# Kernel optimization log

Hardware: AMD Instinct MI355X
Metric: run time of the kernel (lower is better)

Reference implementation:

```python
import jax, jax.numpy as jnp
import numpy as np

THRESHOLD = 0.5

def _conv(x, w, b):
    y = jax.lax.conv_general_dilated(x, w, (1, 1), 'SAME',
                                     dimension_numbers=('NCHW', 'OIHW', 'NCHW'))
    return y + b[None, :, None, None]

def _gather2d(img, iy, ix):
    # img [B,C,H,W], iy/ix [B,h,w] int -> [B,C,h,w]
    return jax.vmap(lambda im, y, x: im[:, y, x])(img, iy, ix)

def _grid_sample_bilinear(img, grid):
    # torch F.grid_sample(mode='bilinear', padding_mode='border', align_corners=False)
    # img [B,C,H,W], grid [B,h,w,2] with (x,y) in [-1,1]
    B, C, H, W = img.shape
    x = (grid[..., 0] + 1.0) * (W * 0.5) - 0.5
    y = (grid[..., 1] + 1.0) * (H * 0.5) - 0.5
    x0 = jnp.floor(x); y0 = jnp.floor(y)
    wx = (x - x0)[:, None, :, :]; wy = (y - y0)[:, None, :, :]
    x0i = jnp.clip(x0.astype(jnp.int32), 0, W - 1)
    x1i = jnp.clip(x0.astype(jnp.int32) + 1, 0, W - 1)
    y0i = jnp.clip(y0.astype(jnp.int32), 0, H - 1)
    y1i = jnp.clip(y0.astype(jnp.int32) + 1, 0, H - 1)
    v00 = _gather2d(img, y0i, x0i); v01 = _gather2d(img, y0i, x1i)
    v10 = _gather2d(img, y1i, x0i); v11 = _gather2d(img, y1i, x1i)
    return (v00 * (1 - wx) * (1 - wy) + v01 * wx * (1 - wy)
            + v10 * (1 - wx) * wy + v11 * wx * wy)

def _encoder(lr, w_in, b_in, res_w, res_b):
    x = _conv(lr, w_in, b_in)
    for i in range(res_w.shape[0]):  # small fixed layer count
        r = _conv(jax.nn.relu(_conv(x, res_w[i, 0], res_b[i, 0])), res_w[i, 1], res_b[i, 1])
        x = x + r
    return x  # [B,64,Hl,Wl]

def _make_inp(feat, coord, cell):
    # nearest-sampled feature + relative coord + scaled cell (LIIF-style make_inp)
    B, C, Hl, Wl = feat.shape
    y = (coord[..., 0] + 1.0) * (Hl * 0.5) - 0.5
    x = (coord[..., 1] + 1.0) * (Wl * 0.5) - 0.5
    iyn = jnp.clip(jnp.floor(y + 0.5).astype(jnp.int32), 0, Hl - 1)
    ixn = jnp.clip(jnp.floor(x + 0.5).astype(jnp.int32), 0, Wl - 1)
    fs = _gather2d(feat, iyn, ixn).transpose(0, 2, 3, 1)  # [B,h,w,C]
    cy = (2.0 * iyn + 1.0) / Hl - 1.0
    cx = (2.0 * ixn + 1.0) / Wl - 1.0
    rel = jnp.stack([(coord[..., 0] - cy) * Hl, (coord[..., 1] - cx) * Wl], axis=-1)
    cell_s = cell * jnp.array([Hl, Wl], dtype=cell.dtype)
    return jnp.concatenate([fs, rel, cell_s], axis=-1)  # [B,h,w,C+4]

def setup_inputs() -> dict:
    key = jax.random.key(0)
    ks = jax.random.split(key, 16)
    B, Hl, Wl, h, w, C = 2, 96, 96, 384, 384, 64
    lr = jax.random.normal(ks[0], (B, 3, Hl, Wl), jnp.float32)
    ys = (jnp.arange(h, dtype=jnp.float32) + 0.5) / h * 2.0 - 1.0
    xs = (jnp.arange(w, dtype=jnp.float32) + 0.5) / w * 2.0 - 1.0
    gy, gx = jnp.meshgrid(ys, xs, indexing='ij')
    coord = jnp.broadcast_to(jnp.stack([gy, gx], -1), (B, h, w, 2))  # (y,x)
    cell = jnp.broadcast_to(jnp.array([2.0 / h, 2.0 / w], jnp.float32), (B, h, w, 2))
    def lin(k, fan_in, shape):
        return jax.random.normal(k, shape, jnp.float32) / np.sqrt(fan_in)
    D = C + 4  # 68
    return {
        'lr': lr, 'coord': coord, 'cell': cell,
        'enc_w_in': jax.random.normal(ks[1], (C, 3, 3, 3), jnp.float32) * 0.05,
        'enc_b_in': jnp.zeros((C,), jnp.float32),
        'enc_res_w': jax.random.normal(ks[2], (4, 2, C, C, 3, 3), jnp.float32) * 0.02,
        'enc_res_b': jnp.zeros((4, 2, C), jnp.float32),
        'cls_w1': lin(ks[3], D, (D, 64)), 'cls_b1': jnp.zeros((64,), jnp.float32),
        'cls_w2': lin(ks[4], 64, (64, 2)), 'cls_b2': jnp.zeros((2,), jnp.float32),
        'lw1': lin(ks[5], D, (D, 64)), 'lb1': jnp.zeros((64,), jnp.float32),
        'lw2': lin(ks[6], 64, (64, 64)), 'lb2': jnp.zeros((64,), jnp.float32),
        'lw3': lin(ks[7], 64, (64, 3)), 'lb3': jnp.zeros((3,), jnp.float32),
        'hw1': lin(ks[8], D, (D, 256)), 'hb1': jnp.zeros((256,), jnp.float32),
        'hmid_w': lin(ks[9], 256, (2, 256, 256)), 'hmid_b': jnp.zeros((2, 256), jnp.float32),
        'hw_out': lin(ks[10], 256, (256, 3)), 'hb_out': jnp.zeros((3,), jnp.float32),
    }

def reference(lr, coord, cell, enc_w_in, enc_b_in, enc_res_w, enc_res_b,
              cls_w1, cls_b1, cls_w2, cls_b2,
              lw1, lb1, lw2, lb2, lw3, lb3,
              hw1, hb1, hmid_w, hmid_b, hw_out, hb_out):
    feat = _encoder(lr, enc_w_in, enc_b_in, enc_res_w, enc_res_b)
    inp = _make_inp(feat, coord, cell)  # [B,h,w,68]
    # classifier -> softmax difficulty gate
    logits = jax.nn.relu(inp @ cls_w1 + cls_b1) @ cls_w2 + cls_b2
    diff = jax.nn.softmax(logits, axis=-1)
    hard = diff[..., 1] > THRESHOLD  # [B,h,w]
    # light sampler (dense over all pixels; where-select == gather/scatter dispatch)
    pl = jax.nn.relu(inp @ lw1 + lb1)
    pl = jax.nn.relu(pl @ lw2 + lb2)
    pl = pl @ lw3 + lb3
    # heavy sampler
    ph = jax.nn.relu(inp @ hw1 + hb1)
    for i in range(hmid_w.shape[0]):
        ph = jax.nn.relu(ph @ hmid_w[i] + hmid_b[i])
    ph = ph @ hw_out + hb_out
    pred = jnp.where(hard[..., None], ph, pl)  # [B,h,w,3]
    pred = pred.transpose(0, 3, 1, 2)  # [B,3,h,w]
    pred = pred + _grid_sample_bilinear(lr, coord[..., ::-1])  # coord.flip(-1) -> (x,y)
    ratio_easy = jnp.mean(1.0 - hard.astype(jnp.float32))
    return (pred, ratio_easy)
```

## Files before the change

kernel.cpp:

```cpp
#include <hip/hip_runtime.h>

#define HL 96
#define WL 96
#define HO 384
#define WO 384
#define NPIX (2*HO*WO)
#define FEAT_ELEMS ((size_t)2*64*HL*WL)
#define PLANE (HL*WL)

typedef unsigned short us4 __attribute__((ext_vector_type(4)));
typedef unsigned short us8 __attribute__((ext_vector_type(8)));
typedef __bf16         b8  __attribute__((ext_vector_type(8)));
typedef float          f32x4 __attribute__((ext_vector_type(4)));

__device__ __forceinline__ unsigned short f2b(float x) {
  unsigned u = __builtin_bit_cast(unsigned, x);
  unsigned r = (u + 0x7FFFu + ((u >> 16) & 1u)) >> 16;
  return (unsigned short)r;
}

__device__ __forceinline__ f32x4 MF(us8 a, us8 b, f32x4 c) {
  return __builtin_amdgcn_mfma_f32_16x16x32_bf16(
      __builtin_bit_cast(b8, a), __builtin_bit_cast(b8, b), c, 0, 0, 0);
}

template<int CIN, int COPT, bool RELU, bool RES>
__global__ __launch_bounds__(256) void conv_s_k(
    const float* __restrict__ in, const float* __restrict__ wP,
    const float* __restrict__ bias, const float* __restrict__ res,
    float* __restrict__ out)
{
  const int t   = threadIdx.x;
  const int p   = blockIdx.x * 256 + t;
  const int co0 = blockIdx.y * COPT;
  const int b   = blockIdx.z;
  const int x   = p % WL;
  const bool xl = (x == 0), xr = (x == WL - 1);

  float acc[COPT];
  #pragma unroll
  for (int j = 0; j < COPT; ++j) acc[j] = bias[co0 + j];

  int  ic[3]; bool yv[3];
  int  im[3], ip[3];
  #pragma unroll
  for (int ky = 0; ky < 3; ++ky) {
    int pr = p + (ky - 1) * WL;
    yv[ky] = ((unsigned)pr < (unsigned)PLANE);
    ic[ky] = yv[ky] ? pr : 0;
    im[ky] = ic[ky] - 1; if (im[ky] < 0) im[ky] = 0;
    ip[ky] = ic[ky] + 1; if (ip[ky] > PLANE - 1) ip[ky] = PLANE - 1;
  }

  const float* inb = in + (size_t)b * CIN * PLANE;

  #pragma unroll 2
  for (int ci = 0; ci < CIN; ++ci) {
    const float* pl = inb + (size_t)ci * PLANE;
    #pragma unroll
    for (int ky = 0; ky < 3; ++ky) {
      float am = pl[im[ky]];
      float a0 = pl[ic[ky]];
      float ap = pl[ip[ky]];
      if (!yv[ky]) { am = 0.f; a0 = 0.f; ap = 0.f; }
      if (xl) am = 0.f;
      if (xr) ap = 0.f;
      const float* wrow = wP + (size_t)(ci * 9 + ky * 3) * 64 + co0;
      #pragma unroll
      for (int j = 0; j < COPT; ++j) acc[j] += am * wrow[j];
      #pragma unroll
      for (int j = 0; j < COPT; ++j) acc[j] += a0 * wrow[64 + j];
      #pragma unroll
      for (int j = 0; j < COPT; ++j) acc[j] += ap * wrow[128 + j];
    }
  }

  size_t ob = ((size_t)b * 64 + co0) * PLANE + p;
  #pragma unroll
  for (int j = 0; j < COPT; ++j) {
    float v = acc[j];
    if (RELU) v = fmaxf(v, 0.f);
    if (RES)  v += res[ob + (size_t)j * PLANE];
    out[ob + (size_t)j * PLANE] = v;
  }
}

__global__ __launch_bounds__(256) void prep_convw_k(const float* __restrict__ src,
                                                    float* __restrict__ dst, int cin)
{
  int idx = blockIdx.x * 256 + threadIdx.x;
  int tot = cin * 9 * 64;
  if (idx >= tot) return;
  int co = idx % 64; int r = idx / 64;
  int ci = r / 9, tap = r % 9;
  dst[idx] = src[((size_t)co * cin + ci) * 9 + tap];
}

__global__ __launch_bounds__(256) void nchw_to_nhwc_k(const float* __restrict__ in,
                                                      float* __restrict__ out)
{
  __shared__ float s[64][65];
  const int b = blockIdx.y;
  const int pix0 = blockIdx.x * 64;
  const int t = threadIdx.x;
  #pragma unroll
  for (int cc = 0; cc < 16; ++cc) {
    int co = cc * 4 + (t >> 6);
    int px = t & 63;
    s[px][co] = in[((size_t)b * 64 + co) * PLANE + pix0 + px];
  }
  __syncthreads();
  #pragma unroll
  for (int pp = 0; pp < 16; ++pp) {
    int px = pp * 4 + (t >> 6);
    int co = t & 63;
    out[((size_t)b * PLANE + pix0 + px) * 64 + co] = s[px][co];
  }
}

__global__ __launch_bounds__(256) void prep_wt_k(const float* __restrict__ src,
    unsigned short* __restrict__ dst, int K, int N, int Kpad, int Npad)
{
  int idx = blockIdx.x * 256 + threadIdx.x;
  if (idx >= Kpad * Npad) return;
  int n = idx / Kpad, k = idx - n * Kpad;
  float v = (k < K && n < N) ? src[(size_t)k * N + n] : 0.f;
  dst[idx] = f2b(v);
}

template<int NT, int KT>
__device__ __forceinline__ void mfma_compute(
    const unsigned short* __restrict__ aBase, int AS,
    const unsigned short* __restrict__ WT, int Kpad,
    int n0, int lane, f32x4 (&acc)[4][NT])
{
  const int lr = lane & 15;
  const int lc = lane >> 4;
  #pragma unroll
  for (int m = 0; m < 4; ++m)
    #pragma unroll
    for (int j = 0; j < NT; ++j) acc[m][j] = (f32x4){0.f, 0.f, 0.f, 0.f};

  const unsigned short* aP = aBase + lr * AS + lc * 8;
  const unsigned short* bP = WT + (size_t)(n0 + lr) * Kpad + lc * 8;

  constexpr int KCH = (KT >= 4) ? 4 : KT;
  #pragma unroll
  for (int kc = 0; kc < KT; kc += KCH) {
    us8 breg[KCH][NT];
    #pragma unroll
    for (int kk = 0; kk < KCH; ++kk)
      #pragma unroll
      for (int j = 0; j < NT; ++j)
        breg[kk][j] = *(const us8*)(bP + (size_t)j * 16 * Kpad + (kc + kk) * 32);
    #pragma unroll
    for (int kc2 = 0; kc2 < KCH; ++kc2) {
      us8 a0[4];
      #pragma unroll
      for (int m = 0; m < 4; ++m)
        a0[m] = *(const us8*)(aP + (m * 16) * AS + (kc + kc2) * 32);
      #pragma unroll
      for (int m = 0; m < 4; ++m)
        #pragma unroll
        for (int j = 0; j < NT; ++j)
          acc[m][j] = MF(a0[m], breg[kc2][j], acc[m][j]);
    }
  }
}

template<int NT, bool RELU>
__device__ __forceinline__ void mfma_store(
    const f32x4 (&acc)[4][NT], const float* __restrict__ bias,
    unsigned short* __restrict__ dBase, int DS, int dCol0, int n0, int lane)
{
  const int lr = lane & 15;
  const int lc = lane >> 4;
  #pragma unroll
  for (int j = 0; j < NT; ++j) {
    int n = n0 + j * 16 + lr;
    float bv = bias[n];
    #pragma unroll
    for (int m = 0; m < 4; ++m)
      #pragma unroll
      for (int r = 0; r < 4; ++r) {
        float v = acc[m][j][r] + bv;
        if (RELU) v = fmaxf(v, 0.f);
        dBase[(m * 16 + lc * 4 + r) * DS + dCol0 + n] = f2b(v);
      }
  }
}

template<int KT>
__device__ __forceinline__ void mfma_out3w(
    const unsigned short* __restrict__ aBase, int AS,
    const unsigned short* __restrict__ WT, int Kpad,
    const float* __restrict__ bias, float (*dst)[4], int mtile, int lane)
{
  const int lr = lane & 15;
  const int lc = lane >> 4;
  f32x4 acc = (f32x4){0.f, 0.f, 0.f, 0.f};
  const unsigned short* aP = aBase + (mtile * 16 + lr) * AS + lc * 8;
  const unsigned short* bP = WT + (size_t)lr * Kpad + lc * 8;

  constexpr int KCH = (KT >= 4) ? 4 : KT;
  #pragma unroll
  for (int kc = 0; kc < KT; kc += KCH) {
    us8 breg[KCH];
    #pragma unroll
    for (int kk = 0; kk < KCH; ++kk)
      breg[kk] = *(const us8*)(bP + (kc + kk) * 32);
    #pragma unroll
    for (int kk = 0; kk < KCH; ++kk) {
      us8 a = *(const us8*)(aP + (kc + kk) * 32);
      acc = MF(a, breg[kk], acc);
    }
  }
  if (lr < 3) {
    float bv = bias[lr];
    #pragma unroll
    for (int r = 0; r < 4; ++r)
      dst[mtile * 16 + lc * 4 + r][lr] = acc[r] + bv;
  }
}

__device__ __forceinline__ void nearest_idx(float gy, float gx, int& iy, int& ix)
{
  float fy = (gy + 1.f) * (HL * 0.5f) - 0.5f;
  float fx = (gx + 1.f) * (WL * 0.5f) - 0.5f;
  iy = min(max((int)floorf(fy + 0.5f), 0), HL - 1);
  ix = min(max((int)floorf(fx + 0.5f), 0), WL - 1);
}

__device__ __forceinline__ float bilinear_lr(const float* __restrict__ lrimg,
                                             int b, int ch, float gy, float gx)
{
  float x = (gx + 1.f) * (WL * 0.5f) - 0.5f;
  float y = (gy + 1.f) * (HL * 0.5f) - 0.5f;
  float xf = floorf(x), yf = floorf(y);
  float wx = x - xf, wy = y - yf;
  int x0i = min(max((int)xf,     0), WL - 1);
  int x1i = min(max((int)xf + 1, 0), WL - 1);
  int y0i = min(max((int)yf,     0), HL - 1);
  int y1i = min(max((int)yf + 1, 0), HL - 1);
  const float* img = lrimg + ((size_t)b * 3 + ch) * PLANE;
  float v00 = img[y0i * WL + x0i], v01 = img[y0i * WL + x1i];
  float v10 = img[y1i * WL + x0i], v11 = img[y1i * WL + x1i];
  return v00 * (1.f - wx) * (1.f - wy) + v01 * wx * (1.f - wy)
       + v10 * (1.f - wx) * wy + v11 * wx * wy;
}

template<int JB>
__device__ __forceinline__ void cls_block(
    const float* __restrict__ fp,
    float e0, float e1, float e2, float e3,
    const float* __restrict__ cw1, const float* __restrict__ cb1,
    const float* __restrict__ cw2,
    int j0, float& l0, float& l1)
{
  float acc[JB];
  #pragma unroll
  for (int j = 0; j < JB; ++j) acc[j] = cb1[j0 + j];
  #pragma unroll 4
  for (int kq = 0; kq < 16; ++kq) {
    float4 a4 = *(const float4*)(fp + kq * 4);
    float av[4] = {a4.x, a4.y, a4.z, a4.w};
    #pragma unroll
    for (int kk = 0; kk < 4; ++kk) {
      const float* wr = cw1 + (size_t)(kq * 4 + kk) * 64 + j0;
      float a = av[kk];
      #pragma unroll
      for (int j = 0; j < JB; ++j) acc[j] += a * wr[j];
    }
  }
  {
    const float* wr = cw1 + (size_t)64 * 64 + j0;
    #pragma unroll
    for (int j = 0; j < JB; ++j) acc[j] += e0 * wr[j];
    wr += 64;
    #pragma unroll
    for (int j = 0; j < JB; ++j) acc[j] += e1 * wr[j];
    wr += 64;
    #pragma unroll
    for (int j = 0; j < JB; ++j) acc[j] += e2 * wr[j];
    wr += 64;
    #pragma unroll
    for (int j = 0; j < JB; ++j) acc[j] += e3 * wr[j];
  }
  #pragma unroll
  for (int j = 0; j < JB; ++j) {
    float h = fmaxf(acc[j], 0.f);
    l0 += h * cw2[(j0 + j) * 2 + 0];
    l1 += h * cw2[(j0 + j) * 2 + 1];
  }
}

__global__ __launch_bounds__(256, 4) void cls_gate_k(
    const float* __restrict__ featT, const float* __restrict__ coord,
    const float* __restrict__ cell,
    const float* __restrict__ cw1, const float* __restrict__ cb1,
    const float* __restrict__ cw2, const float* __restrict__ cb2,
    int* __restrict__ counters, unsigned* __restrict__ easyList,
    unsigned* __restrict__ hardList)
{
  const int g = blockIdx.x * 256 + threadIdx.x;
  const int b = g / (HO * WO);
  const float gy = coord[(size_t)g * 2 + 0];
  const float gx = coord[(size_t)g * 2 + 1];
  int iy, ix; nearest_idx(gy, gx, iy, ix);
  const float* fp = featT + (((size_t)b * PLANE) + iy * WL + ix) * 64;

  float cy = (2.f * iy + 1.f) / HL - 1.f;
  float cx = (2.f * ix + 1.f) / WL - 1.f;
  float e0 = (gy - cy) * HL;
  float e1 = (gx - cx) * WL;
  float e2 = cell[(size_t)g * 2 + 0] * HL;
  float e3 = cell[(size_t)g * 2 + 1] * WL;

  float l0 = cb2[0], l1 = cb2[1];
  cls_block<32>(fp, e0, e1, e2, e3, cw1, cb1, cw2, 0,  l0, l1);
  cls_block<32>(fp, e0, e1, e2, e3, cw1, cb1, cw2, 32, l0, l1);
  bool hard = (l1 > l0);

  unsigned long long mh = __ballot(hard);
  int lane = threadIdx.x & 63;
  int nh = __popcll(mh);
  int baseH = 0, baseE = 0;
  if (lane == 0) {
    baseH = atomicAdd(&counters[1], nh);
    baseE = atomicAdd(&counters[0], 64 - nh);
  }
  baseH = __shfl(baseH, 0);
  baseE = __shfl(baseE, 0);
  unsigned long long below = (1ull << lane) - 1ull;
  int hb = __popcll(mh & below);
  if (hard) hardList[baseH + hb] = (unsigned)g;
  else      easyList[baseE + (lane - hb)] = (unsigned)g;
}

__device__ __forceinline__ void build_inp_row(
    const float* __restrict__ featT, const float* __restrict__ coord,
    const float* __restrict__ cell, unsigned g, int p, int q8,
    unsigned short (*sInpB)[104])
{
  int b = g / (HO * WO);
  float gy = coord[(size_t)g * 2 + 0];
  float gx = coord[(size_t)g * 2 + 1];
  int iy, ix; nearest_idx(gy, gx, iy, ix);
  const float* fpt = featT + (((size_t)b * PLANE) + iy * WL + ix) * 64 + q8 * 8;
  float4 u0 = *(const float4*)fpt;
  float4 u1 = *(const float4*)(fpt + 4);
  us8 pk;
  pk[0]=f2b(u0.x); pk[1]=f2b(u0.y); pk[2]=f2b(u0.z); pk[3]=f2b(u0.w);
  pk[4]=f2b(u1.x); pk[5]=f2b(u1.y); pk[6]=f2b(u1.z); pk[7]=f2b(u1.w);
  *(us8*)&sInpB[p][q8 * 8] = pk;
  if (q8 == 0) {
    float cy = (2.f * iy + 1.f) / HL - 1.f;
    float cx = (2.f * ix + 1.f) / WL - 1.f;
    float e0 = (gy - cy) * HL, e1 = (gx - cx) * WL;
    float e2 = cell[(size_t)g * 2 + 0] * HL, e3 = cell[(size_t)g * 2 + 1] * WL;
    us4 pe; pe[0]=f2b(e0); pe[1]=f2b(e1); pe[2]=f2b(e2); pe[3]=f2b(e3);
    *(us4*)&sInpB[p][64] = pe;
  }
  if (q8 == 1) {
    us4 z = (us4){0,0,0,0};
    #pragma unroll
    for (int c = 0; c < 9; ++c) *(us4*)&sInpB[p][68 + c * 4] = z;
  }
}

__global__ __launch_bounds__(256, 4) void light_k(
    const float* __restrict__ featT, const float* __restrict__ coord,
    const float* __restrict__ cell,  const float* __restrict__ lrimg,
    const float* __restrict__ lb1, const float* __restrict__ lb2,
    const float* __restrict__ lb3,
    const unsigned short* __restrict__ lw1T, const unsigned short* __restrict__ lw2T,
    const unsigned short* __restrict__ lw3T,
    const int* __restrict__ counters, const unsigned* __restrict__ list,
    float* __restrict__ out)
{
  const int nE = counters[0];
  const int g0 = blockIdx.x * 64;
  if (g0 >= nE) return;

  __shared__ unsigned short sInpB[64][104];
  __shared__ unsigned short sL1[64][72];
  __shared__ unsigned short sL2[64][72];
  __shared__ float sP[64][4];
  __shared__ unsigned sIdx[64];

  const int t = threadIdx.x, lane = t & 63, w = t >> 6;

  {
    const int p = t >> 2, q = t & 3;
    int i = g0 + p; if (i > nE - 1) i = nE - 1;
    unsigned g = list[i];
    if (q == 0) sIdx[p] = g;
    build_inp_row(featT, coord, cell, g, p, q * 2,     sInpB);
    build_inp_row(featT, coord, cell, g, p, q * 2 + 1, sInpB);
  }
  __syncthreads();

  { f32x4 acc[4][1];
    mfma_compute<1, 3>(&sInpB[0][0], 104, lw1T, 96, w * 16, lane, acc);
    mfma_store<1, true>(acc, lb1, &sL1[0][0], 72, 0, w * 16, lane); }
  __syncthreads();
  { f32x4 acc[4][1];
    mfma_compute<1, 2>(&sL1[0][0], 72, lw2T, 64, w * 16, lane, acc);
    mfma_store<1, true>(acc, lb2, &sL2[0][0], 72, 0, w * 16, lane); }
  __syncthreads();
  mfma_out3w<2>(&sL2[0][0], 72, lw3T, 64, lb3, sP, w, lane);
  __syncthreads();

  if (t < 192) {
    int p = t / 3, ch = t % 3;
    int i = g0 + p;
    if (i < nE) {
      unsigned g = sIdx[p];
      int b = g / (HO * WO);
      int rem = g % (HO * WO);
      int oy = rem / WO, ox = rem % WO;
      float gy = coord[(size_t)g * 2 + 0];
      float gx = coord[(size_t)g * 2 + 1];
      float v = bilinear_lr(lrimg, b, ch, gy, gx);
      out[(((size_t)b * 3 + ch) * HO + oy) * WO + ox] = sP[p][ch] + v;
    }
  }
}

__global__ __launch_bounds__(512, 4) void heavy_k(
    const float* __restrict__ featT, const float* __restrict__ coord,
    const float* __restrict__ cell,  const float* __restrict__ lrimg,
    const float* __restrict__ hb1, const float* __restrict__ hmb,
    const float* __restrict__ hbo,
    const unsigned short* __restrict__ hw1T, const unsigned short* __restrict__ hm0T,
    const unsigned short* __restrict__ hm1T, const unsigned short* __restrict__ hwoT,
    const int* __restrict__ counters, const unsigned* __restrict__ list,
    float* __restrict__ out)
{
  const int nH = counters[1];
  const int g0 = blockIdx.x * 64;
  if (g0 >= nH) return;

  __shared__ unsigned short sAct[64][264];
  __shared__ unsigned short sInpB[64][104];
  __shared__ float sP[64][4];
  __shared__ unsigned sIdx[64];

  const int t = threadIdx.x, lane = t & 63, w = t >> 6;

  {
    const int p = t >> 3, q = t & 7;
    int i = g0 + p; if (i > nH - 1) i = nH - 1;
    unsigned g = list[i];
    if (q == 0) sIdx[p] = g;
    build_inp_row(featT, coord, cell, g, p, q, sInpB);
  }
  __syncthreads();

  { f32x4 acc[4][2];
    mfma_compute<2, 3>(&sInpB[0][0], 104, hw1T, 96, w * 32, lane, acc);
    mfma_store<2, true>(acc, hb1, &sAct[0][0], 264, 0, w * 32, lane); }
  __syncthreads();
  { f32x4 acc[4][2];
    mfma_compute<2, 8>(&sAct[0][0], 264, hm0T, 256, w * 32, lane, acc);
    __syncthreads();
    mfma_store<2, true>(acc, hmb, &sAct[0][0], 264, 0, w * 32, lane); }
  __syncthreads();
  { f32x4 acc[4][2];
    mfma_compute<2, 8>(&sAct[0][0], 264, hm1T, 256, w * 32, lane, acc);
    __syncthreads();
    mfma_store<2, true>(acc, hmb + 256, &sAct[0][0], 264, 0, w * 32, lane); }
  __syncthreads();
  if (w < 4) mfma_out3w<8>(&sAct[0][0], 264, hwoT, 256, hbo, sP, w, lane);
  __syncthreads();

  if (t < 192) {
    int p = t / 3, ch = t % 3;
    int i = g0 + p;
    if (i < nH) {
      unsigned g = sIdx[p];
      int b = g / (HO * WO);
      int rem = g % (HO * WO);
      int oy = rem / WO, ox = rem % WO;
      float gy = coord[(size_t)g * 2 + 0];
      float gx = coord[(size_t)g * 2 + 1];
      float v = bilinear_lr(lrimg, b, ch, gy, gx);
      out[(((size_t)b * 3 + ch) * HO + oy) * WO + ox] = sP[p][ch] + v;
    }
  }
}

__global__ void finalize_k(const int* __restrict__ counters, float* __restrict__ out)
{
  out[(size_t)NPIX * 3] = (float)(counters[0]) / (float)NPIX;
}

extern "C" void kernel_launch(void* const* d_in, const int* in_sizes, int n_in,
                              void* d_out, int out_size, void* d_ws, size_t ws_size,
                              hipStream_t stream)
{
  const float* lr       = (const float*)d_in[0];
  const float* coord    = (const float*)d_in[1];
  const float* cell     = (const float*)d_in[2];
  const float* enc_w_in = (const float*)d_in[3];
  const float* enc_b_in = (const float*)d_in[4];
  const float* enc_rw   = (const float*)d_in[5];
  const float* enc_rb   = (const float*)d_in[6];
  const float* cw1      = (const float*)d_in[7];
  const float* cb1      = (const float*)d_in[8];
  const float* cw2      = (const float*)d_in[9];
  const float* cb2      = (const float*)d_in[10];
  const float* lw1      = (const float*)d_in[11];
  const float* lb1      = (const float*)d_in[12];
  const float* lw2      = (const float*)d_in[13];
  const float* lb2      = (const float*)d_in[14];
  const float* lw3      = (const float*)d_in[15];
  const float* lb3      = (const float*)d_in[16];
  const float* hw1      = (const float*)d_in[17];
  const float* hb1      = (const float*)d_in[18];
  const float* hmw      = (const float*)d_in[19];
  const float* hmb      = (const float*)d_in[20];
  const float* hwo      = (const float*)d_in[21];
  const float* hbo      = (const float*)d_in[22];
  float* out = (float*)d_out;

  char* ws = (char*)d_ws;
  float* xA    = (float*)(ws + 1024);
  float* tmp   = xA  + FEAT_ELEMS;
  float* xB    = tmp + FEAT_ELEMS;
  float* featT = tmp;
  unsigned short* wb = (unsigned short*)(xB + FEAT_ELEMS);
  unsigned short* lw1T = wb;
  unsigned short* lw2T = lw1T + 64*96;
  unsigned short* lw3T = lw2T + 64*64;
  unsigned short* hw1T = lw3T + 16*64;
  unsigned short* hm0T = hw1T + 256*96;
  unsigned short* hm1T = hm0T + 65536;
  unsigned short* hwoT = hm1T + 65536;
  const size_t nb16 = 64*96 + 64*64 + 16*64 + 256*96 + 2*65536 + 16*256;
  float* cwIn  = (float*)(wb + nb16);
  float* cwRes = cwIn + 1728;
  size_t need = 1024 + 3 * FEAT_ELEMS * sizeof(float)
              + nb16 * 2 + (1728 + 8 * 36864) * sizeof(float);
  if (ws_size < need) return;

  int*      counters = (int*)xB;
  unsigned* easyList = (unsigned*)(xB + 16);
  unsigned* hardList = easyList + NPIX;

  auto prep = [&](const float* s, unsigned short* d, int K, int N, int Kp, int Np) {
    int tot = Kp * Np;
    prep_wt_k<<<(tot + 255) / 256, 256, 0, stream>>>(s, d, K, N, Kp, Np);
  };
  prep(lw1, lw1T, 68, 64, 96, 64);
  prep(lw2, lw2T, 64, 64, 64, 64);
  prep(lw3, lw3T, 64, 3, 64, 16);
  prep(hw1, hw1T, 68, 256, 96, 256);
  prep(hmw,         hm0T, 256, 256, 256, 256);
  prep(hmw + 65536, hm1T, 256, 256, 256, 256);
  prep(hwo, hwoT, 256, 3, 256, 16);

  prep_convw_k<<<(1728 + 255) / 256, 256, 0, stream>>>(enc_w_in, cwIn, 3);
  for (int l = 0; l < 8; ++l)
    prep_convw_k<<<(36864 + 255) / 256, 256, 0, stream>>>(
        enc_rw + (size_t)l * 36864, cwRes + (size_t)l * 36864, 64);

  dim3 cgrid(36, 16, 2);
  conv_s_k<3, 4, false, false><<<cgrid, 256, 0, stream>>>(lr, cwIn, enc_b_in, nullptr, xA);

  float* cur = xA; float* oth = xB;
  for (int i = 0; i < 4; ++i) {
    const float* wp0 = cwRes + (size_t)(2 * i)     * 36864;
    const float* wp1 = cwRes + (size_t)(2 * i + 1) * 36864;
    const float* b0 = enc_rb + i * 128;
    const float* b1 = b0 + 64;
    conv_s_k<64, 4, true,  false><<<cgrid, 256, 0, stream>>>(cur, wp0, b0, nullptr, tmp);
    conv_s_k<64, 4, false, true ><<<cgrid, 256, 0, stream>>>(tmp, wp1, b1, cur, oth);
    float* sw2 = cur; cur = oth; oth = sw2;
  }

  nchw_to_nhwc_k<<<dim3(144, 2), 256, 0, stream>>>(cur, featT);

  hipMemsetAsync(counters, 0, 16, stream);

  cls_gate_k<<<NPIX / 256, 256, 0, stream>>>(featT, coord, cell,
      cw1, cb1, cw2, cb2, counters, easyList, hardList);

  light_k<<<NPIX / 64, 256, 0, stream>>>(featT, coord, cell, lr,
      lb1, lb2, lb3, lw1T, lw2T, lw3T, counters, easyList, out);

  heavy_k<<<NPIX / 64, 512, 0, stream>>>(featT, coord, cell, lr,
      hb1, hmb, hbo, hw1T, hm0T, hm1T, hwoT, counters, hardList, out);

  finalize_k<<<1, 1, 0, stream>>>(counters, out);
}
```

Measured before the change: 690.1 us.

## Split residual convs over input-channel halves with 4-pixel register tiles

Each residual-block 3x3 conv now has every thread compute four adjacent output pixels per row with float4 loads, so the neighbouring input values are reused in registers. The input channels are split into two halves run as separate grid slices, which write partial sums to two new buffers. A vectorized combine kernel then adds the halves and applies ReLU or the residual. This aims to cut redundant input loads and keep enough parallelism, at the cost of two extra feature-sized buffers and an extra pass over memory per conv.

Result: slower. 817.1 us (+18.4%).

```diff
diff --git a/kernel.cpp b/kernel.cpp
--- a/kernel.cpp
+++ b/kernel.cpp
@@ -83,6 +83,102 @@
     if (RES)  v += res[ob + (size_t)j * PLANE];
     out[ob + (size_t)j * PLANE] = v;
   }
+}
+
+template<int CIH>
+__global__ __launch_bounds__(256) void conv4_s_k(
+    const float* __restrict__ in, const float* __restrict__ wP,
+    const float* __restrict__ bias,
+    float* __restrict__ pA, float* __restrict__ pB)
+{
+  const int t    = threadIdx.x;
+  const int quad = blockIdx.x * 256 + t;
+  const int y    = quad / 24;
+  const int x0   = (quad % 24) * 4;
+  const int co0  = blockIdx.y * 4;
+  const int z    = blockIdx.z;
+  const int b    = z >> 1;
+  const int half = z & 1;
+  float* outp    = half ? pB : pA;
+  const bool xL  = (x0 == 0);
+  const bool xR  = (x0 == WL - 4);
+
+  float acc[4][4];
+  #pragma unroll
+  for (int p = 0; p < 4; ++p)
+    #pragma unroll
+    for (int j = 0; j < 4; ++j) acc[p][j] = (half == 0) ? bias[co0 + j] * (p == p) : 0.f;
+  if (half == 0) {
+    #pragma unroll
+    for (int p = 0; p < 4; ++p)
+      #pragma unroll
+      for (int j = 0; j < 4; ++j) acc[p][j] = bias[co0 + j];
+  } else {
+    #pragma unroll
+    for (int p = 0; p < 4; ++p)
+      #pragma unroll
+      for (int j = 0; j < 4; ++j) acc[p][j] = 0.f;
+  }
+
+  int  rowOff[3]; bool rv[3];
+  #pragma unroll
+  for (int rr = 0; rr < 3; ++rr) {
+    int ry = y - 1 + rr;
+    rv[rr] = (ry >= 0 && ry < HL);
+    rowOff[rr] = (rv[rr] ? ry : 0) * WL;
+  }
+
+  const float* inb = in + ((size_t)b * 64 + half * CIH) * PLANE;
+  const float* wPh = wP + (size_t)(half * CIH) * 9 * 64;
+
+  for (int ci = 0; ci < CIH; ++ci) {
+    const float* pl = inb + (size_t)ci * PLANE;
+    #pragma unroll
+    for (int ky = 0; ky < 3; ++ky) {
+      const float* row = pl + rowOff[ky];
+      float4 m = *(const float4*)(row + x0);
+      float vL = xL ? 0.f : row[x0 - 1];
+      float vR = xR ? 0.f : row[x0 + 4];
+      if (!rv[ky]) { m.x = 0.f; m.y = 0.f; m.z = 0.f; m.w = 0.f; vL = 0.f; vR = 0.f; }
+      const float* wrow = wPh + (size_t)(ci * 9 + ky * 3) * 64 + co0;
+      #pragma unroll
+      for (int j = 0; j < 4; ++j) {
+        float w0 = wrow[j], w1 = wrow[64 + j], w2 = wrow[128 + j];
+        acc[0][j] += vL  * w0; acc[0][j] += m.x * w1; acc[0][j] += m.y * w2;
+        acc[1][j] += m.x * w0; acc[1][j] += m.y * w1; acc[1][j] += m.z * w2;
+        acc[2][j] += m.y * w0; acc[2][j] += m.z * w1; acc[2][j] += m.w * w2;
+        acc[3][j] += m.z * w0; acc[3][j] += m.w * w1; acc[3][j] += vR  * w2;
+      }
+    }
+  }
+
+  size_t ob = ((size_t)b * 64 + co0) * PLANE + y * WL + x0;
+  #pragma unroll
+  for (int j = 0; j < 4; ++j) {
+    float4 v; v.x = acc[0][j]; v.y = acc[1][j]; v.z = acc[2][j]; v.w = acc[3][j];
+    *(float4*)(outp + ob + (size_t)j * PLANE) = v;
+  }
+}
+
+template<bool RELU, bool RES>
+__global__ __launch_bounds__(256) void combine_k(
+    const float* __restrict__ pA, const float* __restrict__ pB,
+    const float* __restrict__ res, float* __restrict__ out)
+{
+  size_t i = ((size_t)blockIdx.x * 256 + threadIdx.x) * 4;
+  float4 a = *(const float4*)(pA + i);
+  float4 b = *(const float4*)(pB + i);
+  float4 v;
+  v.x = a.x + b.x; v.y = a.y + b.y; v.z = a.z + b.z; v.w = a.w + b.w;
+  if (RELU) {
+    v.x = fmaxf(v.x, 0.f); v.y = fmaxf(v.y, 0.f);
+    v.z = fmaxf(v.z, 0.f); v.w = fmaxf(v.w, 0.f);
+  }
+  if (RES) {
+    float4 r = *(const float4*)(res + i);
+    v.x += r.x; v.y += r.y; v.z += r.z; v.w += r.w;
+  }
+  *(float4*)(out + i) = v;
 }
 
 __global__ __launch_bounds__(256) void prep_convw_k(const float* __restrict__ src,
@@ -528,8 +624,10 @@
   float* xA    = (float*)(ws + 1024);
   float* tmp   = xA  + FEAT_ELEMS;
   float* xB    = tmp + FEAT_ELEMS;
+  float* pA    = xB  + FEAT_ELEMS;
+  float* pB    = pA  + FEAT_ELEMS;
   float* featT = tmp;
-  unsigned short* wb = (unsigned short*)(xB + FEAT_ELEMS);
+  unsigned short* wb = (unsigned short*)(pB + FEAT_ELEMS);
   unsigned short* lw1T = wb;
   unsigned short* lw2T = lw1T + 64*96;
   unsigned short* lw3T = lw2T + 64*64;
@@ -540,7 +638,7 @@
   const size_t nb16 = 64*96 + 64*64 + 16*64 + 256*96 + 2*65536 + 16*256;
   float* cwIn  = (float*)(wb + nb16);
   float* cwRes = cwIn + 1728;
-  size_t need = 1024 + 3 * FEAT_ELEMS * sizeof(float)
+  size_t need = 1024 + 5 * FEAT_ELEMS * sizeof(float)
               + nb16 * 2 + (1728 + 8 * 36864) * sizeof(float);
   if (ws_size < need) return;
 
@@ -565,8 +663,11 @@
     prep_convw_k<<<(36864 + 255) / 256, 256, 0, stream>>>(
         enc_rw + (size_t)l * 36864, cwRes + (size_t)l * 36864, 64);
 
-  dim3 cgrid(36, 16, 2);
-  conv_s_k<3, 4, false, false><<<cgrid, 256, 0, stream>>>(lr, cwIn, enc_b_in, nullptr, xA);
+  dim3 cgrid1(36, 16, 2);
+  dim3 cgrid4(9, 16, 4);
+  const int combGrid = (int)(FEAT_ELEMS / 4 / 256);
+
+  conv_s_k<3, 4, false, false><<<cgrid1, 256, 0, stream>>>(lr, cwIn, enc_b_in, nullptr, xA);
 
   float* cur = xA; float* oth = xB;
   for (int i = 0; i < 4; ++i) {
@@ -574,8 +675,10 @@
     const float* wp1 = cwRes + (size_t)(2 * i + 1) * 36864;
     const float* b0 = enc_rb + i * 128;
     const float* b1 = b0 + 64;
-    conv_s_k<64, 4, true,  false><<<cgrid, 256, 0, stream>>>(cur, wp0, b0, nullptr, tmp);
-    conv_s_k<64, 4, false, true ><<<cgrid, 256, 0, stream>>>(tmp, wp1, b1, cur, oth);
+    conv4_s_k<32><<<cgrid4, 256, 0, stream>>>(cur, wp0, b0, pA, pB);
+    combine_k<true, false><<<combGrid, 256, 0, stream>>>(pA, pB, nullptr, tmp);
+    conv4_s_k<32><<<cgrid4, 256, 0, stream>>>(tmp, wp1, b1, pA, pB);
+    combine_k<false, true><<<combGrid, 256, 0, stream>>>(pA, pB, cur, oth);
     float* sw2 = cur; cur = oth; oth = sw2;
   }
 
```
